# Performance work log

Measured on AMD Instinct MI355X. Metric: run time of the kernel, lower is better.

## Reference

```python
import jax, jax.numpy as jnp
import numpy as np

N, E = 100000, 1280000
IN_D, FEAT, HID, OUT = 256, 64, 64, 64
NEG_SLOPE = 0.2


def _gat_conv(x, src, dst, w, a_s, a_d, b, n):
    # x: [N, in], w: [in, out], a_s/a_d/b: [out]; edges src->dst (messages flow to dst)
    h = x @ w                                   # [N, out]
    e = jax.nn.leaky_relu((h @ a_s)[src] + (h @ a_d)[dst], NEG_SLOPE)  # [E]
    m = jax.ops.segment_max(e, dst, num_segments=n)                     # scatter-softmax (stable)
    ex = jnp.exp(e - m[dst])
    den = jax.ops.segment_sum(ex, dst, num_segments=n)
    alpha = ex / (den[dst] + 1e-16)
    out = jax.ops.segment_sum(alpha[:, None] * h[src], dst, num_segments=n)
    return out + b


def setup_inputs() -> dict:
    key = jax.random.key(0)
    ks = jax.random.split(key, 16)
    rn = lambda k, shape, s=0.05: jax.random.normal(k, shape, jnp.float32) * s
    return {
        'x': jax.random.normal(ks[0], (N, IN_D), jnp.float32),
        'src': jax.random.randint(ks[1], (E,), 0, N),
        'dst': jax.random.randint(ks[2], (E,), 0, N),
        'lin_w': rn(ks[3], (IN_D, FEAT)), 'lin_b': jnp.zeros((FEAT,), jnp.float32),
        'w1': rn(ks[4], (FEAT, HID)), 'a1s': rn(ks[5], (HID,)), 'a1d': rn(ks[6], (HID,)), 'b1': jnp.zeros((HID,), jnp.float32),
        'w2': rn(ks[7], (HID, HID)), 'a2s': rn(ks[8], (HID,)), 'a2d': rn(ks[9], (HID,)), 'b2': jnp.zeros((HID,), jnp.float32),
        'w3': rn(ks[10], (HID, OUT)), 'a3s': rn(ks[11], (OUT,)), 'a3d': rn(ks[12], (OUT,)), 'b3': jnp.zeros((OUT,), jnp.float32),
    }


def reference(x, src, dst, lin_w, lin_b, w1, a1s, a1d, b1, w2, a2s, a2d, b2, w3, a3s, a3d, b3):
    n = x.shape[0]
    loop = jnp.arange(n, dtype=src.dtype)        # GATConv add_self_loops=True
    s = jnp.concatenate([src, loop])
    d = jnp.concatenate([dst, loop])
    h = x @ lin_w + lin_b                        # feature_pre linear
    h = jax.nn.relu(_gat_conv(h, s, d, w1, a1s, a1d, b1, n))  # dropout is identity in eval
    h = jax.nn.relu(_gat_conv(h, s, d, w2, a2s, a2d, b2, n))
    h = _gat_conv(h, s, d, w3, a3s, a3d, b3, n)
    norm = jnp.linalg.norm(h, axis=-1, keepdims=True)          # F.normalize(p=2, dim=-1)
    return h / jnp.maximum(norm, 1e-12)
```

## Files before the change

### kernel.cpp

```cpp
#include <hip/hip_runtime.h>


constexpr float NEG_SLOPE = 0.2f;
#define BKT_SHIFT 9
#define BKT_N     512
#define PCHUNK    4096

template <bool DOTS>
__global__ __launch_bounds__(256) void gemm64(
    const float* __restrict__ A, const float* __restrict__ B,
    const float* __restrict__ bias, float* __restrict__ C, int M, int K,
    const float* __restrict__ a_s, const float* __restrict__ a_d,
    float* __restrict__ hs, float* __restrict__ hd)
{
    __shared__ float As[16][64];
    __shared__ float Bs[16][64];
    const int tid  = threadIdx.x;
    const int row0 = blockIdx.x * 64;
    const int tr = tid >> 4;
    const int tc = tid & 15;
    const int ar = tid >> 2;
    const int ak = (tid & 3) << 2;
    const int bk = tid >> 4;
    const int bc = (tid & 15) << 2;

    float acc[4][4] = {};

    for (int k0 = 0; k0 < K; k0 += 16) {
        float4 av = make_float4(0.f, 0.f, 0.f, 0.f);
        const int arow = row0 + ar;
        if (arow < M) av = *(const float4*)(A + (size_t)arow * K + k0 + ak);
        const float4 bv = *(const float4*)(B + (size_t)(k0 + bk) * 64 + bc);
        __syncthreads();
        As[ak + 0][ar] = av.x;
        As[ak + 1][ar] = av.y;
        As[ak + 2][ar] = av.z;
        As[ak + 3][ar] = av.w;
        *(float4*)(&Bs[bk][bc]) = bv;
        __syncthreads();
        #pragma unroll
        for (int kk = 0; kk < 16; ++kk) {
            const float4 a4 = *(const float4*)(&As[kk][tr << 2]);
            const float4 b4 = *(const float4*)(&Bs[kk][tc << 2]);
            const float aa[4] = {a4.x, a4.y, a4.z, a4.w};
            const float bb[4] = {b4.x, b4.y, b4.z, b4.w};
            #pragma unroll
            for (int i = 0; i < 4; ++i)
                #pragma unroll
                for (int j = 0; j < 4; ++j)
                    acc[i][j] = fmaf(aa[i], bb[j], acc[i][j]);
        }
    }

    const int c = tc << 2;
    float b0 = 0.f, b1 = 0.f, b2 = 0.f, b3 = 0.f;
    if (bias) { b0 = bias[c]; b1 = bias[c + 1]; b2 = bias[c + 2]; b3 = bias[c + 3]; }
    #pragma unroll
    for (int i = 0; i < 4; ++i) {
        const int r = row0 + (tr << 2) + i;
        if (r < M) {
            float4 v;
            v.x = acc[i][0] + b0;
            v.y = acc[i][1] + b1;
            v.z = acc[i][2] + b2;
            v.w = acc[i][3] + b3;
            *(float4*)(C + (size_t)r * 64 + c) = v;
        }
    }

    if (DOTS) {
        const float4 asv = *(const float4*)(a_s + c);
        const float4 adv = *(const float4*)(a_d + c);
        #pragma unroll
        for (int i = 0; i < 4; ++i) {
            float sdot = acc[i][0] * asv.x + acc[i][1] * asv.y +
                         acc[i][2] * asv.z + acc[i][3] * asv.w;
            float ddot = acc[i][0] * adv.x + acc[i][1] * adv.y +
                         acc[i][2] * adv.z + acc[i][3] * adv.w;
            #pragma unroll
            for (int off = 1; off < 16; off <<= 1) {
                sdot += __shfl_xor(sdot, off);
                ddot += __shfl_xor(ddot, off);
            }
            const int r = row0 + (tr << 2) + i;
            if (tc == 0 && r < M) { hs[r] = sdot; hd[r] = ddot; }
        }
    }
}

__global__ __launch_bounds__(256) void edge_hist(
    const int* __restrict__ dst, int* __restrict__ cnt, int e)
{
    const int i = blockIdx.x * blockDim.x + threadIdx.x;
    if (i < e) atomicAdd(&cnt[dst[i]], 1);
}

__global__ __launch_bounds__(256) void scan1(
    const int* __restrict__ cnt, int* __restrict__ out,
    int* __restrict__ bsum, int n)
{
    __shared__ int wsum[4];
    const int tid  = threadIdx.x;
    const int lane = tid & 63;
    const int w    = tid >> 6;
    const int base = blockIdx.x * 1024;
    int vals[4];
    int tsum = 0;
    #pragma unroll
    for (int i = 0; i < 4; ++i) {
        const int idx = base + tid * 4 + i;
        vals[i] = (idx < n) ? cnt[idx] : 0;
        tsum += vals[i];
    }
    int x = tsum;
    #pragma unroll
    for (int off = 1; off < 64; off <<= 1) {
        const int y = __shfl_up(x, off);
        if (lane >= off) x += y;
    }
    if (lane == 63) wsum[w] = x;
    __syncthreads();
    int wofs = 0;
    for (int k = 0; k < w; ++k) wofs += wsum[k];
    int excl = wofs + x - tsum;
    #pragma unroll
    for (int i = 0; i < 4; ++i) {
        const int idx = base + tid * 4 + i;
        if (idx < n) out[idx] = excl;
        excl += vals[i];
    }
    if (tid == 255) bsum[blockIdx.x] = wofs + x;
}

__global__ __launch_bounds__(128) void scan2(int* __restrict__ b, int nb)
{
    __shared__ int wtot[2];
    const int tid = threadIdx.x;
    const int lane = tid & 63;
    const int w = tid >> 6;
    const int v = (tid < nb) ? b[tid] : 0;
    int x = v;
    #pragma unroll
    for (int off = 1; off < 64; off <<= 1) {
        const int y = __shfl_up(x, off);
        if (lane >= off) x += y;
    }
    if (lane == 63) wtot[w] = x;
    __syncthreads();
    const int add = (w == 1) ? wtot[0] : 0;
    if (tid < nb) b[tid] = add + x - v;
}

__global__ __launch_bounds__(256) void scan3(
    int* __restrict__ out, const int* __restrict__ bsum, int n, int total)
{
    const int idx = blockIdx.x * blockDim.x + threadIdx.x;
    if (idx < n) out[idx] += bsum[idx >> 10];
    if (idx == 0) out[n] = total;
}

__global__ __launch_bounds__(256) void cursor_init(
    const int* __restrict__ offs, int* __restrict__ gcur, int n, int nb)
{
    const int b = threadIdx.x;
    if (b < nb) gcur[b] = offs[min(b << BKT_SHIFT, n)];
}

__global__ __launch_bounds__(256) void edge_partition(
    const int* __restrict__ src, const int* __restrict__ dst,
    int* __restrict__ gcursor, int2* __restrict__ pairs, int e, int nb)
{
    __shared__ int2 stage[PCHUNK];
    __shared__ int lcnt[256];
    __shared__ int lstart[256];
    __shared__ int lfill[256];
    __shared__ int gbase[256];
    __shared__ int wsum[4];

    const int tid  = threadIdx.x;
    const int lane = tid & 63;
    const int w    = tid >> 6;
    const int base = blockIdx.x * PCHUNK;
    const int cnt_here = min(PCHUNK, e - base);

    lcnt[tid] = 0; lfill[tid] = 0;
    __syncthreads();

    int2 items[PCHUNK / 256];
    int nmine = 0;
    for (int i = tid; i < cnt_here; i += 256) {
        int2 it; it.x = src[base + i]; it.y = dst[base + i];
        items[nmine++] = it;
        atomicAdd(&lcnt[it.y >> BKT_SHIFT], 1);
    }
    __syncthreads();

    const int v = lcnt[tid];
    int x = v;
    #pragma unroll
    for (int off = 1; off < 64; off <<= 1) {
        const int y = __shfl_up(x, off);
        if (lane >= off) x += y;
    }
    if (lane == 63) wsum[w] = x;
    __syncthreads();
    int carry = 0;
    for (int k = 0; k < w; ++k) carry += wsum[k];
    lstart[tid] = carry + x - v;
    if (tid < nb && v > 0) gbase[tid] = atomicAdd(&gcursor[tid], v);
    __syncthreads();

    for (int k = 0; k < nmine; ++k) {
        const int b = items[k].y >> BKT_SHIFT;
        const int p = lstart[b] + atomicAdd(&lfill[b], 1);
        stage[p] = items[k];
    }
    __syncthreads();

    for (int s = tid; s < cnt_here; s += 256) {
        const int2 it = stage[s];
        const int b = it.y >> BKT_SHIFT;
        pairs[gbase[b] + (s - lstart[b])] = it;
    }
}

__global__ __launch_bounds__(256) void bucket_scatter(
    const int2* __restrict__ pairs, const int* __restrict__ offs,
    int* __restrict__ ssrc, int n)
{
    __shared__ int pos[BKT_N];
    const int node0 = blockIdx.x << BKT_SHIFT;
    const int node1 = min(n, node0 + BKT_N);
    const int tid = threadIdx.x;
    for (int i = tid; i < node1 - node0; i += 256) pos[i] = offs[node0 + i];
    __syncthreads();
    const int e0 = offs[node0];
    const int e1 = offs[node1];
    for (int j = e0 + tid; j < e1; j += 256) {
        const int2 it = pairs[j];
        const int p = atomicAdd(&pos[it.y - node0], 1);
        ssrc[p] = it.x;
    }
}

template <int MODE>
__global__ __launch_bounds__(256) void gat_agg(
    const float* __restrict__ hp, const float* __restrict__ hs,
    const float* __restrict__ hd, const int* __restrict__ offs,
    const int* __restrict__ ssrc, const float* __restrict__ bias,
    float* __restrict__ out, int n)
{
    const int wid  = (blockIdx.x * blockDim.x + threadIdx.x) >> 6;
    const int lane = threadIdx.x & 63;
    if (wid >= n) return;
    const int sub = lane >> 4;
    const int fl  = (lane & 15) << 2;

    const float hdi = hd[wid];
    float den = 0.f;
    float4 acc = make_float4(0.f, 0.f, 0.f, 0.f);

    if (sub == 0) {
        float e = hs[wid] + hdi;
        e = (e > 0.f) ? e : NEG_SLOPE * e;
        const float ex = __expf(e);
        const float4 hv = *(const float4*)(hp + (size_t)wid * 64 + fl);
        den = ex;
        acc.x = ex * hv.x; acc.y = ex * hv.y;
        acc.z = ex * hv.z; acc.w = ex * hv.w;
    }

    const int start = offs[wid];
    const int end   = offs[wid + 1];
    #pragma unroll 2
    for (int j = start + sub; j < end; j += 4) {
        const int s = ssrc[j];
        float e2 = hs[s] + hdi;
        e2 = (e2 > 0.f) ? e2 : NEG_SLOPE * e2;
        const float ex2 = __expf(e2);
        const float4 hv = *(const float4*)(hp + (size_t)s * 64 + fl);
        den += ex2;
        acc.x = fmaf(ex2, hv.x, acc.x);
        acc.y = fmaf(ex2, hv.y, acc.y);
        acc.z = fmaf(ex2, hv.z, acc.z);
        acc.w = fmaf(ex2, hv.w, acc.w);
    }

    den   += __shfl_xor(den, 16);   den   += __shfl_xor(den, 32);
    acc.x += __shfl_xor(acc.x, 16); acc.x += __shfl_xor(acc.x, 32);
    acc.y += __shfl_xor(acc.y, 16); acc.y += __shfl_xor(acc.y, 32);
    acc.z += __shfl_xor(acc.z, 16); acc.z += __shfl_xor(acc.z, 32);
    acc.w += __shfl_xor(acc.w, 16); acc.w += __shfl_xor(acc.w, 32);

    const float4 bv = *(const float4*)(bias + fl);
    const float inv = 1.f / (den + 1e-16f);
    float4 v;
    v.x = acc.x * inv + bv.x;
    v.y = acc.y * inv + bv.y;
    v.z = acc.z * inv + bv.z;
    v.w = acc.w * inv + bv.w;

    if (MODE == 0) {
        v.x = fmaxf(v.x, 0.f); v.y = fmaxf(v.y, 0.f);
        v.z = fmaxf(v.z, 0.f); v.w = fmaxf(v.w, 0.f);
    } else {
        float sq = v.x * v.x + v.y * v.y + v.z * v.z + v.w * v.w;
        #pragma unroll
        for (int off = 1; off < 16; off <<= 1) sq += __shfl_xor(sq, off);
        const float s = 1.f / fmaxf(sqrtf(sq), 1e-12f);
        v.x *= s; v.y *= s; v.z *= s; v.w *= s;
    }
    if (sub == 0) *(float4*)(out + (size_t)wid * 64 + fl) = v;
}

extern "C" void kernel_launch(void* const* d_in, const int* in_sizes, int n_in,
                              void* d_out, int out_size, void* d_ws, size_t ws_size,
                              hipStream_t stream)
{
    const float* x     = (const float*)d_in[0];
    const int*   src   = (const int*)d_in[1];
    const int*   dst   = (const int*)d_in[2];
    const float* lin_w = (const float*)d_in[3];
    const float* lin_b = (const float*)d_in[4];
    const float* w1  = (const float*)d_in[5];
    const float* a1s = (const float*)d_in[6];
    const float* a1d = (const float*)d_in[7];
    const float* b1  = (const float*)d_in[8];
    const float* w2  = (const float*)d_in[9];
    const float* a2s = (const float*)d_in[10];
    const float* a2d = (const float*)d_in[11];
    const float* b2  = (const float*)d_in[12];
    const float* w3  = (const float*)d_in[13];
    const float* a3s = (const float*)d_in[14];
    const float* a3d = (const float*)d_in[15];
    const float* b3  = (const float*)d_in[16];

    const int n = in_sizes[0] / 256;
    const int E = in_sizes[1];
    const int nb = (n + BKT_N - 1) >> BKT_SHIFT;

    char* wsp = (char*)d_ws;
    auto alloc = [&](size_t bytes) -> void* {
        void* p = (void*)wsp;
        wsp += (bytes + 255) & ~(size_t)255;
        return p;
    };
    float* bufA = (float*)alloc((size_t)n * 64 * sizeof(float));
    float* bufB = (float*)alloc((size_t)n * 64 * sizeof(float));
    float* hs   = (float*)alloc((size_t)n * sizeof(float));
    float* hd   = (float*)alloc((size_t)n * sizeof(float));
    int*   offs = (int*)alloc((size_t)(n + 1) * sizeof(int));
    int*   cnt  = (int*)alloc((size_t)n * sizeof(int));
    int*   bsum = (int*)alloc(1024 * sizeof(int));
    int*   gcur = (int*)alloc(256 * sizeof(int));
    int*   ssrc = (int*)alloc((size_t)E * sizeof(int));
    int2*  pairs = (int2*)bufB;

    const int edgeBlocks = (E + 255) / 256;
    const int nodeWaveBlocks = (n + 3) / 4;
    const int gemmBlocks = (n + 63) / 64;
    const int nScanBlocks = (n + 1023) / 1024;
    const int partBlocks = (E + PCHUNK - 1) / PCHUNK;

    hipMemsetAsync(cnt, 0, (size_t)n * sizeof(int), stream);
    edge_hist<<<edgeBlocks, 256, 0, stream>>>(dst, cnt, E);
    scan1<<<nScanBlocks, 256, 0, stream>>>(cnt, offs, bsum, n);
    scan2<<<1, 128, 0, stream>>>(bsum, nScanBlocks);
    scan3<<<(n + 255) / 256, 256, 0, stream>>>(offs, bsum, n, E);
    cursor_init<<<1, 256, 0, stream>>>(offs, gcur, n, nb);
    edge_partition<<<partBlocks, 256, 0, stream>>>(src, dst, gcur, pairs, E, nb);
    bucket_scatter<<<nb, 256, 0, stream>>>(pairs, offs, ssrc, n);

    gemm64<false><<<gemmBlocks, 256, 0, stream>>>(x, lin_w, lin_b, bufA, n, 256,
                                                  nullptr, nullptr, nullptr, nullptr);

    gemm64<true><<<gemmBlocks, 256, 0, stream>>>(bufA, w1, nullptr, bufB, n, 64,
                                                 a1s, a1d, hs, hd);
    gat_agg<0><<<nodeWaveBlocks, 256, 0, stream>>>(bufB, hs, hd, offs, ssrc, b1, bufA, n);

    gemm64<true><<<gemmBlocks, 256, 0, stream>>>(bufA, w2, nullptr, bufB, n, 64,
                                                 a2s, a2d, hs, hd);
    gat_agg<0><<<nodeWaveBlocks, 256, 0, stream>>>(bufB, hs, hd, offs, ssrc, b2, bufA, n);

    gemm64<true><<<gemmBlocks, 256, 0, stream>>>(bufA, w3, nullptr, bufB, n, 64,
                                                 a3s, a3d, hs, hd);
    gat_agg<1><<<nodeWaveBlocks, 256, 0, stream>>>(bufB, hs, hd, offs, ssrc, b3,
                                                   (float*)d_out, n);
}
```

Before: 539.9 us.

## Store node features in bf16 and use MFMA bf16 GEMMs

Replaces the fp32 SIMT GEMMs with MFMA 16x16x32 bf16 kernels using pre-transposed bf16 weights, and stores the intermediate node feature buffers in bf16. The aggregation kernel now gathers 8 bf16 features per lane with 8 edges in flight per wave, halving gather bytes per edge. The edge-pair buffer gets its own allocation instead of aliasing bufB. The cost is reduced precision in the features and attention logits inputs, plus an extra weight-prep launch.

Result: faster. 502.6 us (-6.9%).

```diff
diff --git a/kernel.cpp b/kernel.cpp
--- a/kernel.cpp
+++ b/kernel.cpp
@@ -6,86 +6,153 @@
 #define BKT_N     512
 #define PCHUNK    4096
 
-template <bool DOTS>
-__global__ __launch_bounds__(256) void gemm64(
-    const float* __restrict__ A, const float* __restrict__ B,
-    const float* __restrict__ bias, float* __restrict__ C, int M, int K,
+typedef __attribute__((ext_vector_type(8))) short bf16x8;
+typedef __attribute__((ext_vector_type(4))) float f32x4;
+
+__device__ inline ushort f2bf(float x) {
+    union { float f; uint u; } v; v.f = x;
+    return (ushort)((v.u + 0x7FFFu + ((v.u >> 16) & 1u)) >> 16);
+}
+__device__ inline void bf2f(uint u, float& lo, float& hi) {
+    union { uint u; float f; } a, b;
+    a.u = u << 16; b.u = u & 0xFFFF0000u;
+    lo = a.f; hi = b.f;
+}
+__device__ inline uint pk(float a, float b) {
+    return (uint)f2bf(a) | ((uint)f2bf(b) << 16);
+}
+
+__global__ __launch_bounds__(256) void prep_w(
+    const float* __restrict__ lw, const float* __restrict__ w1,
+    const float* __restrict__ w2, const float* __restrict__ w3,
+    ushort* __restrict__ lwT, ushort* __restrict__ w1T,
+    ushort* __restrict__ w2T, ushort* __restrict__ w3T)
+{
+    const int i = blockIdx.x * 256 + threadIdx.x;
+    if (i < 64 * 256) {
+        const int nn = i >> 8, k = i & 255;
+        lwT[i] = f2bf(lw[k * 64 + nn]);
+    } else {
+        const int j = i - 64 * 256;
+        if (j < 4096) {
+            const int nn = j >> 6, k = j & 63;
+            w1T[j] = f2bf(w1[k * 64 + nn]);
+            w2T[j] = f2bf(w2[k * 64 + nn]);
+            w3T[j] = f2bf(w3[k * 64 + nn]);
+        }
+    }
+}
+
+__global__ __launch_bounds__(256) void gemm_pre(
+    const float* __restrict__ x, const ushort* __restrict__ lwT,
+    const float* __restrict__ bias, ushort* __restrict__ C, int M)
+{
+    __shared__ __align__(16) ushort ctile[4][16][64];
+    const int tid = threadIdx.x;
+    const int w = tid >> 6, lane = tid & 63;
+    const int rw0 = (blockIdx.x * 4 + w) * 16;
+    if (rw0 >= M) return;
+    const int c = lane & 15, q = lane >> 4;
+
+    f32x4 acc[4];
+    #pragma unroll
+    for (int t = 0; t < 4; ++t) acc[t] = (f32x4){0.f, 0.f, 0.f, 0.f};
+
+    const float* ap = x + (size_t)(rw0 + c) * 256 + q * 8;
+    #pragma unroll
+    for (int s = 0; s < 8; ++s) {
+        const float4 p0 = *(const float4*)(ap + s * 32);
+        const float4 p1 = *(const float4*)(ap + s * 32 + 4);
+        bf16x8 af;
+        af[0] = (short)f2bf(p0.x); af[1] = (short)f2bf(p0.y);
+        af[2] = (short)f2bf(p0.z); af[3] = (short)f2bf(p0.w);
+        af[4] = (short)f2bf(p1.x); af[5] = (short)f2bf(p1.y);
+        af[6] = (short)f2bf(p1.z); af[7] = (short)f2bf(p1.w);
+        #pragma unroll
+        for (int t = 0; t < 4; ++t) {
+            const bf16x8 bf = *(const bf16x8*)(lwT + (size_t)(t * 16 + c) * 256 + s * 32 + q * 8);
+            acc[t] = __builtin_amdgcn_mfma_f32_16x16x32_bf16(af, bf, acc[t], 0, 0, 0);
+        }
+    }
+
+    #pragma unroll
+    for (int t = 0; t < 4; ++t) {
+        const float bv = bias[t * 16 + c];
+        #pragma unroll
+        for (int r = 0; r < 4; ++r)
+            ctile[w][q * 4 + r][t * 16 + c] = f2bf(acc[t][r] + bv);
+    }
+    const int row = lane >> 2, eo = (lane & 3) * 16;
+    const uint4 v0 = *(const uint4*)(&ctile[w][row][eo]);
+    const uint4 v1 = *(const uint4*)(&ctile[w][row][eo + 8]);
+    *(uint4*)(C + (size_t)(rw0 + row) * 64 + eo)     = v0;
+    *(uint4*)(C + (size_t)(rw0 + row) * 64 + eo + 8) = v1;
+}
+
+__global__ __launch_bounds__(256) void gemm_layer(
+    const ushort* __restrict__ A, const ushort* __restrict__ WT,
     const float* __restrict__ a_s, const float* __restrict__ a_d,
-    float* __restrict__ hs, float* __restrict__ hd)
-{
-    __shared__ float As[16][64];
-    __shared__ float Bs[16][64];
-    const int tid  = threadIdx.x;
-    const int row0 = blockIdx.x * 64;
-    const int tr = tid >> 4;
-    const int tc = tid & 15;
-    const int ar = tid >> 2;
-    const int ak = (tid & 3) << 2;
-    const int bk = tid >> 4;
-    const int bc = (tid & 15) << 2;
-
-    float acc[4][4] = {};
-
-    for (int k0 = 0; k0 < K; k0 += 16) {
-        float4 av = make_float4(0.f, 0.f, 0.f, 0.f);
-        const int arow = row0 + ar;
-        if (arow < M) av = *(const float4*)(A + (size_t)arow * K + k0 + ak);
-        const float4 bv = *(const float4*)(B + (size_t)(k0 + bk) * 64 + bc);
-        __syncthreads();
-        As[ak + 0][ar] = av.x;
-        As[ak + 1][ar] = av.y;
-        As[ak + 2][ar] = av.z;
-        As[ak + 3][ar] = av.w;
-        *(float4*)(&Bs[bk][bc]) = bv;
-        __syncthreads();
-        #pragma unroll
-        for (int kk = 0; kk < 16; ++kk) {
-            const float4 a4 = *(const float4*)(&As[kk][tr << 2]);
-            const float4 b4 = *(const float4*)(&Bs[kk][tc << 2]);
-            const float aa[4] = {a4.x, a4.y, a4.z, a4.w};
-            const float bb[4] = {b4.x, b4.y, b4.z, b4.w};
-            #pragma unroll
-            for (int i = 0; i < 4; ++i)
-                #pragma unroll
-                for (int j = 0; j < 4; ++j)
-                    acc[i][j] = fmaf(aa[i], bb[j], acc[i][j]);
-        }
-    }
-
-    const int c = tc << 2;
-    float b0 = 0.f, b1 = 0.f, b2 = 0.f, b3 = 0.f;
-    if (bias) { b0 = bias[c]; b1 = bias[c + 1]; b2 = bias[c + 2]; b3 = bias[c + 3]; }
-    #pragma unroll
-    for (int i = 0; i < 4; ++i) {
-        const int r = row0 + (tr << 2) + i;
-        if (r < M) {
-            float4 v;
-            v.x = acc[i][0] + b0;
-            v.y = acc[i][1] + b1;
-            v.z = acc[i][2] + b2;
-            v.w = acc[i][3] + b3;
-            *(float4*)(C + (size_t)r * 64 + c) = v;
-        }
-    }
-
-    if (DOTS) {
-        const float4 asv = *(const float4*)(a_s + c);
-        const float4 adv = *(const float4*)(a_d + c);
-        #pragma unroll
-        for (int i = 0; i < 4; ++i) {
-            float sdot = acc[i][0] * asv.x + acc[i][1] * asv.y +
-                         acc[i][2] * asv.z + acc[i][3] * asv.w;
-            float ddot = acc[i][0] * adv.x + acc[i][1] * adv.y +
-                         acc[i][2] * adv.z + acc[i][3] * adv.w;
-            #pragma unroll
-            for (int off = 1; off < 16; off <<= 1) {
-                sdot += __shfl_xor(sdot, off);
-                ddot += __shfl_xor(ddot, off);
-            }
-            const int r = row0 + (tr << 2) + i;
-            if (tc == 0 && r < M) { hs[r] = sdot; hd[r] = ddot; }
-        }
-    }
+    ushort* __restrict__ C, float* __restrict__ hs, float* __restrict__ hd, int M)
+{
+    __shared__ __align__(16) ushort ctile[4][16][64];
+    const int tid = threadIdx.x;
+    const int w = tid >> 6, lane = tid & 63;
+    const int rw0 = (blockIdx.x * 4 + w) * 16;
+    if (rw0 >= M) return;
+    const int c = lane & 15, q = lane >> 4;
+
+    const ushort* ap = A + (size_t)(rw0 + c) * 64 + q * 8;
+    const bf16x8 a0 = *(const bf16x8*)(ap);
+    const bf16x8 a1 = *(const bf16x8*)(ap + 32);
+
+    f32x4 acc[4];
+    #pragma unroll
+    for (int t = 0; t < 4; ++t) {
+        const ushort* bp = WT + (size_t)(t * 16 + c) * 64 + q * 8;
+        const bf16x8 b0 = *(const bf16x8*)(bp);
+        const bf16x8 b1 = *(const bf16x8*)(bp + 32);
+        f32x4 a = (f32x4){0.f, 0.f, 0.f, 0.f};
+        a = __builtin_amdgcn_mfma_f32_16x16x32_bf16(a0, b0, a, 0, 0, 0);
+        a = __builtin_amdgcn_mfma_f32_16x16x32_bf16(a1, b1, a, 0, 0, 0);
+        acc[t] = a;
+    }
+
+    float ps[4] = {0.f, 0.f, 0.f, 0.f}, pd[4] = {0.f, 0.f, 0.f, 0.f};
+    #pragma unroll
+    for (int t = 0; t < 4; ++t) {
+        const float as = a_s[t * 16 + c], ad = a_d[t * 16 + c];
+        #pragma unroll
+        for (int r = 0; r < 4; ++r) {
+            ps[r] = fmaf(acc[t][r], as, ps[r]);
+            pd[r] = fmaf(acc[t][r], ad, pd[r]);
+        }
+    }
+    #pragma unroll
+    for (int r = 0; r < 4; ++r) {
+        #pragma unroll
+        for (int off = 1; off < 16; off <<= 1) {
+            ps[r] += __shfl_xor(ps[r], off);
+            pd[r] += __shfl_xor(pd[r], off);
+        }
+    }
+    if (c == 0) {
+        #pragma unroll
+        for (int r = 0; r < 4; ++r) {
+            hs[rw0 + q * 4 + r] = ps[r];
+            hd[rw0 + q * 4 + r] = pd[r];
+        }
+    }
+
+    #pragma unroll
+    for (int t = 0; t < 4; ++t)
+        #pragma unroll
+        for (int r = 0; r < 4; ++r)
+            ctile[w][q * 4 + r][t * 16 + c] = f2bf(acc[t][r]);
+    const int row = lane >> 2, eo = (lane & 3) * 16;
+    const uint4 v0 = *(const uint4*)(&ctile[w][row][eo]);
+    const uint4 v1 = *(const uint4*)(&ctile[w][row][eo + 8]);
+    *(uint4*)(C + (size_t)(rw0 + row) * 64 + eo)     = v0;
+    *(uint4*)(C + (size_t)(rw0 + row) * 64 + eo + 8) = v1;
 }
 
 __global__ __launch_bounds__(256) void edge_hist(
@@ -245,72 +312,91 @@
 
 template <int MODE>
 __global__ __launch_bounds__(256) void gat_agg(
-    const float* __restrict__ hp, const float* __restrict__ hs,
+    const ushort* __restrict__ hp, const float* __restrict__ hs,
     const float* __restrict__ hd, const int* __restrict__ offs,
     const int* __restrict__ ssrc, const float* __restrict__ bias,
-    float* __restrict__ out, int n)
+    void* __restrict__ outv, int n)
 {
     const int wid  = (blockIdx.x * blockDim.x + threadIdx.x) >> 6;
     const int lane = threadIdx.x & 63;
     if (wid >= n) return;
-    const int sub = lane >> 4;
-    const int fl  = (lane & 15) << 2;
+    const int sub = lane >> 3;
+    const int f0  = (lane & 7) * 8;
 
     const float hdi = hd[wid];
     float den = 0.f;
-    float4 acc = make_float4(0.f, 0.f, 0.f, 0.f);
+    float acc[8] = {};
 
     if (sub == 0) {
         float e = hs[wid] + hdi;
         e = (e > 0.f) ? e : NEG_SLOPE * e;
         const float ex = __expf(e);
-        const float4 hv = *(const float4*)(hp + (size_t)wid * 64 + fl);
+        const uint4 t = *(const uint4*)(hp + (size_t)wid * 64 + f0);
+        float f[8];
+        bf2f(t.x, f[0], f[1]); bf2f(t.y, f[2], f[3]);
+        bf2f(t.z, f[4], f[5]); bf2f(t.w, f[6], f[7]);
         den = ex;
-        acc.x = ex * hv.x; acc.y = ex * hv.y;
-        acc.z = ex * hv.z; acc.w = ex * hv.w;
+        #pragma unroll
+        for (int i = 0; i < 8; ++i) acc[i] = ex * f[i];
     }
 
     const int start = offs[wid];
     const int end   = offs[wid + 1];
     #pragma unroll 2
-    for (int j = start + sub; j < end; j += 4) {
+    for (int j = start + sub; j < end; j += 8) {
         const int s = ssrc[j];
         float e2 = hs[s] + hdi;
         e2 = (e2 > 0.f) ? e2 : NEG_SLOPE * e2;
         const float ex2 = __expf(e2);
-        const float4 hv = *(const float4*)(hp + (size_t)s * 64 + fl);
+        const uint4 t = *(const uint4*)(hp + (size_t)s * 64 + f0);
+        float f[8];
+        bf2f(t.x, f[0], f[1]); bf2f(t.y, f[2], f[3]);
+        bf2f(t.z, f[4], f[5]); bf2f(t.w, f[6], f[7]);
         den += ex2;
-        acc.x = fmaf(ex2, hv.x, acc.x);
-        acc.y = fmaf(ex2, hv.y, acc.y);
-        acc.z = fmaf(ex2, hv.z, acc.z);
-        acc.w = fmaf(ex2, hv.w, acc.w);
-    }
-
-    den   += __shfl_xor(den, 16);   den   += __shfl_xor(den, 32);
-    acc.x += __shfl_xor(acc.x, 16); acc.x += __shfl_xor(acc.x, 32);
-    acc.y += __shfl_xor(acc.y, 16); acc.y += __shfl_xor(acc.y, 32);
-    acc.z += __shfl_xor(acc.z, 16); acc.z += __shfl_xor(acc.z, 32);
-    acc.w += __shfl_xor(acc.w, 16); acc.w += __shfl_xor(acc.w, 32);
-
-    const float4 bv = *(const float4*)(bias + fl);
+        #pragma unroll
+        for (int i = 0; i < 8; ++i) acc[i] = fmaf(ex2, f[i], acc[i]);
+    }
+
+    #pragma unroll
+    for (int off = 8; off < 64; off <<= 1) {
+        den += __shfl_xor(den, off);
+        #pragma unroll
+        for (int i = 0; i < 8; ++i) acc[i] += __shfl_xor(acc[i], off);
+    }
+
+    const float4 bv0 = *(const float4*)(bias + f0);
+    const float4 bv1 = *(const float4*)(bias + f0 + 4);
+    const float bb[8] = {bv0.x, bv0.y, bv0.z, bv0.w, bv1.x, bv1.y, bv1.z, bv1.w};
     const float inv = 1.f / (den + 1e-16f);
-    float4 v;
-    v.x = acc.x * inv + bv.x;
-    v.y = acc.y * inv + bv.y;
-    v.z = acc.z * inv + bv.z;
-    v.w = acc.w * inv + bv.w;
+    float v[8];
+    #pragma unroll
+    for (int i = 0; i < 8; ++i) v[i] = acc[i] * inv + bb[i];
 
     if (MODE == 0) {
-        v.x = fmaxf(v.x, 0.f); v.y = fmaxf(v.y, 0.f);
-        v.z = fmaxf(v.z, 0.f); v.w = fmaxf(v.w, 0.f);
+        #pragma unroll
+        for (int i = 0; i < 8; ++i) v[i] = fmaxf(v[i], 0.f);
+        if (sub == 0) {
+            uint4 o;
+            o.x = pk(v[0], v[1]); o.y = pk(v[2], v[3]);
+            o.z = pk(v[4], v[5]); o.w = pk(v[6], v[7]);
+            *(uint4*)((ushort*)outv + (size_t)wid * 64 + f0) = o;
+        }
     } else {
-        float sq = v.x * v.x + v.y * v.y + v.z * v.z + v.w * v.w;
-        #pragma unroll
-        for (int off = 1; off < 16; off <<= 1) sq += __shfl_xor(sq, off);
+        float sq = 0.f;
+        #pragma unroll
+        for (int i = 0; i < 8; ++i) sq += v[i] * v[i];
+        #pragma unroll
+        for (int off = 1; off < 8; off <<= 1) sq += __shfl_xor(sq, off);
         const float s = 1.f / fmaxf(sqrtf(sq), 1e-12f);
-        v.x *= s; v.y *= s; v.z *= s; v.w *= s;
-    }
-    if (sub == 0) *(float4*)(out + (size_t)wid * 64 + fl) = v;
+        if (sub == 0) {
+            float* op = (float*)outv + (size_t)wid * 64 + f0;
+            float4 o0, o1;
+            o0.x = v[0] * s; o0.y = v[1] * s; o0.z = v[2] * s; o0.w = v[3] * s;
+            o1.x = v[4] * s; o1.y = v[5] * s; o1.z = v[6] * s; o1.w = v[7] * s;
+            *(float4*)(op)     = o0;
+            *(float4*)(op + 4) = o1;
+        }
+    }
 }
 
 extern "C" void kernel_launch(void* const* d_in, const int* in_sizes, int n_in,
@@ -345,16 +431,20 @@
         wsp += (bytes + 255) & ~(size_t)255;
         return p;
     };
-    float* bufA = (float*)alloc((size_t)n * 64 * sizeof(float));
-    float* bufB = (float*)alloc((size_t)n * 64 * sizeof(float));
-    float* hs   = (float*)alloc((size_t)n * sizeof(float));
-    float* hd   = (float*)alloc((size_t)n * sizeof(float));
-    int*   offs = (int*)alloc((size_t)(n + 1) * sizeof(int));
-    int*   cnt  = (int*)alloc((size_t)n * sizeof(int));
-    int*   bsum = (int*)alloc(1024 * sizeof(int));
-    int*   gcur = (int*)alloc(256 * sizeof(int));
-    int*   ssrc = (int*)alloc((size_t)E * sizeof(int));
-    int2*  pairs = (int2*)bufB;
+    ushort* bufA = (ushort*)alloc((size_t)n * 64 * sizeof(ushort));
+    ushort* bufB = (ushort*)alloc((size_t)n * 64 * sizeof(ushort));
+    float*  hs   = (float*)alloc((size_t)n * sizeof(float));
+    float*  hd   = (float*)alloc((size_t)n * sizeof(float));
+    int*    offs = (int*)alloc((size_t)(n + 1) * sizeof(int));
+    int*    cnt  = (int*)alloc((size_t)n * sizeof(int));
+    int*    bsum = (int*)alloc(1024 * sizeof(int));
+    int*    gcur = (int*)alloc(256 * sizeof(int));
+    int*    ssrc = (int*)alloc((size_t)E * sizeof(int));
+    int2*   pairs = (int2*)alloc((size_t)E * sizeof(int2));
+    ushort* lwT = (ushort*)alloc(64 * 256 * sizeof(ushort));
+    ushort* w1T = (ushort*)alloc(64 * 64 * sizeof(ushort));
+    ushort* w2T = (ushort*)alloc(64 * 64 * sizeof(ushort));
+    ushort* w3T = (ushort*)alloc(64 * 64 * sizeof(ushort));
 
     const int edgeBlocks = (E + 255) / 256;
     const int nodeWaveBlocks = (n + 3) / 4;
@@ -362,6 +452,8 @@
     const int nScanBlocks = (n + 1023) / 1024;
     const int partBlocks = (E + PCHUNK - 1) / PCHUNK;
 
+    prep_w<<<(64 * 256 + 4096 + 255) / 256, 256, 0, stream>>>(
+        lin_w, w1, w2, w3, lwT, w1T, w2T, w3T);
     hipMemsetAsync(cnt, 0, (size_t)n * sizeof(int), stream);
     edge_hist<<<edgeBlocks, 256, 0, stream>>>(dst, cnt, E);
     scan1<<<nScanBlocks, 256, 0, stream>>>(cnt, offs, bsum, n);
@@ -371,19 +463,15 @@
     edge_partition<<<partBlocks, 256, 0, stream>>>(src, dst, gcur, pairs, E, nb);
     bucket_scatter<<<nb, 256, 0, stream>>>(pairs, offs, ssrc, n);
 
-    gemm64<false><<<gemmBlocks, 256, 0, stream>>>(x, lin_w, lin_b, bufA, n, 256,
-                                                  nullptr, nullptr, nullptr, nullptr);
-
-    gemm64<true><<<gemmBlocks, 256, 0, stream>>>(bufA, w1, nullptr, bufB, n, 64,
-                                                 a1s, a1d, hs, hd);
+    gemm_pre<<<gemmBlocks, 256, 0, stream>>>(x, lwT, lin_b, bufA, n);
+
+    gemm_layer<<<gemmBlocks, 256, 0, stream>>>(bufA, w1T, a1s, a1d, bufB, hs, hd, n);
     gat_agg<0><<<nodeWaveBlocks, 256, 0, stream>>>(bufB, hs, hd, offs, ssrc, b1, bufA, n);
 
-    gemm64<true><<<gemmBlocks, 256, 0, stream>>>(bufA, w2, nullptr, bufB, n, 64,
-                                                 a2s, a2d, hs, hd);
+    gemm_layer<<<gemmBlocks, 256, 0, stream>>>(bufA, w2T, a2s, a2d, bufB, hs, hd, n);
     gat_agg<0><<<nodeWaveBlocks, 256, 0, stream>>>(bufB, hs, hd, offs, ssrc, b2, bufA, n);
 
-    gemm64<true><<<gemmBlocks, 256, 0, stream>>>(bufA, w3, nullptr, bufB, n, 64,
-                                                 a3s, a3d, hs, hd);
+    gemm_layer<<<gemmBlocks, 256, 0, stream>>>(bufA, w3T, a3s, a3d, bufB, hs, hd, n);
     gat_agg<1><<<nodeWaveBlocks, 256, 0, stream>>>(bufB, hs, hd, offs, ssrc, b3,
-                                                   (float*)d_out, n);
-}
+                                                   d_out, n);
+}
```
